# Kernel tuning notes

Hardware: AMD Instinct MI355X
Metric: run time of the kernel (lower is better)

## Reference

```python
import jax, jax.numpy as jnp
import numpy as np

N_HEADS = 32
N_KV_HEADS = 8
HEAD_DIM = 128
N_QUERY = N_HEADS // N_KV_HEADS  # 4
ROPE_BASE = 10000.0


def _rope_tables(seq_len, head_dim):
    # inv freqs over pairs of channels (Llama-style interleaved complex rotation)
    inv_freq = 1.0 / (ROPE_BASE ** (jnp.arange(0, head_dim, 2, dtype=jnp.float32) / head_dim))
    t = jnp.arange(seq_len, dtype=jnp.float32)
    ang = t[:, None] * inv_freq[None, :]           # [s, d/2]
    return jnp.cos(ang)[None, :, None, :], jnp.sin(ang)[None, :, None, :]  # [1,s,1,d/2]


def _apply_rope(x, cos, sin):
    # x: [b, s, h, d]; consecutive channel pairs are (real, imag)
    xr = x[..., 0::2]
    xi = x[..., 1::2]
    out_r = xr * cos - xi * sin
    out_i = xr * sin + xi * cos
    return jnp.stack([out_r, out_i], axis=-1).reshape(x.shape)


def setup_inputs() -> dict:
    key = jax.random.key(0)
    kx, kq, kk, kv, ko = jax.random.split(key, 5)
    dim = 4096
    kv_dim = N_KV_HEADS * HEAD_DIM
    scale = 0.02
    return {
        "x": jax.random.normal(kx, (2, 2048, dim), dtype=jnp.float32),
        "wq": jax.random.normal(kq, (dim, dim), dtype=jnp.float32) * scale,
        "wk": jax.random.normal(kk, (dim, kv_dim), dtype=jnp.float32) * scale,
        "wv": jax.random.normal(kv, (dim, kv_dim), dtype=jnp.float32) * scale,
        "wo": jax.random.normal(ko, (dim, dim), dtype=jnp.float32) * scale,
    }


def reference(x, wq, wk, wv, wo):
    b, s, _ = x.shape
    xq = (x @ wq).reshape(b, s, N_HEADS, HEAD_DIM)
    xk = (x @ wk).reshape(b, s, N_KV_HEADS, HEAD_DIM)
    xv = (x @ wv).reshape(b, s, N_KV_HEADS, HEAD_DIM)

    cos, sin = _rope_tables(s, HEAD_DIM)
    xq = _apply_rope(xq, cos, sin)
    xk = _apply_rope(xk, cos, sin)

    # GQA without materializing the KV expand: group query heads per kv head.
    qh = xq.reshape(b, s, N_KV_HEADS, N_QUERY, HEAD_DIM)
    scores = jnp.einsum('bsgnd,btgd->bgnst', qh, xk) / jnp.sqrt(
        jnp.asarray(HEAD_DIM, dtype=xq.dtype))  # [b,g,n,s,t]

    # causal mask: -inf above diagonal
    causal = jnp.arange(s)[:, None] >= jnp.arange(s)[None, :]
    scores = jnp.where(causal[None, None, None, :, :], scores, -jnp.inf)

    att = jax.nn.softmax(scores.astype(jnp.float32), axis=-1).astype(xq.dtype)
    out = jnp.einsum('bgnst,btgd->bsgnd', att, xv).reshape(b, s, N_HEADS * HEAD_DIM)
    return out @ wo
```

## Files before the change

kernel.cpp:

```cpp
#include <hip/hip_runtime.h>
#include <hip/hip_bf16.h>

typedef __attribute__((ext_vector_type(8))) short short8;
typedef __attribute__((ext_vector_type(4))) float f32x4;
typedef __attribute__((ext_vector_type(16))) float f32x16;

#define GLD16(gp, lp) __builtin_amdgcn_global_load_lds( \
    (const __attribute__((address_space(1))) unsigned int*)(gp), \
    (__attribute__((address_space(3))) unsigned int*)(lp), 16, 0, 0)

static __device__ __forceinline__ float bf2f(unsigned short u) {
    union { unsigned int i; float f; } v; v.i = ((unsigned int)u) << 16; return v.f;
}
static __device__ __forceinline__ short f2bf(float f) {
    union { float f; unsigned int i; } v; v.f = f;
    unsigned int r = v.i + 0x7FFFu + ((v.i >> 16) & 1u);
    return (short)(r >> 16);
}
static __device__ __forceinline__ unsigned int pack2bf(float lo, float hi) {
    return ((unsigned int)(unsigned short)f2bf(hi) << 16) | (unsigned int)(unsigned short)f2bf(lo);
}
static __device__ __forceinline__ unsigned int cvtpk(float lo, float hi) {
    unsigned int w;
    asm("v_cvt_pk_bf16_f32 %0, %1, %2" : "=v"(w) : "v"(lo), "v"(hi));
    return w;
}

__global__ void cast_f32_bf16(const float* __restrict__ src, short* __restrict__ dst, int n) {
    int i = (blockIdx.x * 256 + threadIdx.x) * 4;
    if (i >= n) return;
    float4 v = *(const float4*)(src + i);
    short4 o;
    o.x = f2bf(v.x); o.y = f2bf(v.y); o.z = f2bf(v.z); o.w = f2bf(v.w);
    *(short4*)(dst + i) = o;
}

__global__ void transpose_cast(const float* __restrict__ src, short* __restrict__ dst,
                               int N, int dstStride) {
    __shared__ float tile[32][33];
    int k0 = blockIdx.x * 32, n0 = blockIdx.y * 32;
    int t = threadIdx.x, c = t & 31, r = t >> 5;
#pragma unroll
    for (int p = 0; p < 4; ++p)
        tile[r + p * 8][c] = src[(size_t)(k0 + r + p * 8) * N + n0 + c];
    __syncthreads();
#pragma unroll
    for (int p = 0; p < 4; ++p)
        dst[(size_t)(n0 + r + p * 8) * dstStride + k0 + c] = f2bf(tile[c][r + p * 8]);
}

__global__ void transpose_v(const short* __restrict__ qkv, short* __restrict__ vt) {
    __shared__ short tile[32][33];
    int s0 = blockIdx.x * 32, d0 = blockIdx.y * 32;
    int bh = blockIdx.z;
    int b = bh >> 3, h = bh & 7;
    const short* src = qkv + (size_t)b * 2048 * 6144 + 5120 + h * 128;
    short* dst = vt + (size_t)bh * 128 * 2048;
    int t = threadIdx.x, c = t & 31, r = t >> 5;
#pragma unroll
    for (int p = 0; p < 4; ++p)
        tile[r + p * 8][c] = src[(size_t)(s0 + r + p * 8) * 6144 + d0 + c];
    __syncthreads();
#pragma unroll
    for (int p = 0; p < 4; ++p)
        dst[(size_t)(d0 + r + p * 8) * 2048 + s0 + c] = tile[c][r + p * 8];
}

__global__ void rope_tables(float* __restrict__ cs) {
    int i = blockIdx.x * 256 + threadIdx.x;
    int s = i >> 6, d2 = i & 63;
    float inv = expf(-9.210340371976184f * (float)(2 * d2) * (1.0f / 128.0f));
    float ang = (float)s * inv;
    float sn, c;
    sincosf(ang, &sn, &c);
    cs[(size_t)i * 2] = c;
    cs[(size_t)i * 2 + 1] = sn;
}

template<int NH>
__global__ void rope_apply(const short* __restrict__ qkv, const float* __restrict__ cs,
                           short* __restrict__ dst, int colOff, float scale) {
    int i = blockIdx.x * 256 + threadIdx.x;
    int d2 = i & 63;
    int t2 = i >> 6;
    int h = t2 % NH;
    int bs = t2 / NH;
    int s = bs & 2047;
    int b = bs >> 11;
    unsigned int pr = *(const unsigned int*)(qkv + (size_t)bs * 6144 + colOff + h * 128 + 2 * d2);
    float xr = bf2f((unsigned short)(pr & 0xFFFFu));
    float xi = bf2f((unsigned short)(pr >> 16));
    const float* cp = cs + ((size_t)s * 64 + d2) * 2;
    float c = cp[0], sn = cp[1];
    float outr = (xr * c - xi * sn) * scale;
    float outi = (xr * sn + xi * c) * scale;
    *(unsigned int*)(dst + ((size_t)(b * NH + h) * 2048 + s) * 128 + 2 * d2) = pack2bf(outr, outi);
}

template<bool BF16OUT>
__global__ __launch_bounds__(512, 1) void gemm256(const short* __restrict__ A,
                                                  const short* __restrict__ Bt,
                                                  void* __restrict__ Cv,
                                                  int Mtiles, int N, int K) {
    extern __shared__ __align__(16) short lds[];
    short* As = lds;
    short* Bs = lds + 32768;
    const int tid = threadIdx.x;
    const int lane = tid & 63;
    const int wid = tid >> 6;
    const int l31 = lane & 31;
    const int hi = lane >> 5;
    const int wr = wid >> 2;
    const int wc = wid & 3;

    const int nwg = gridDim.x;
    const int id = blockIdx.x;
    const int sid = (id & 7) * (nwg >> 3) + (id >> 3);
    const int m0 = (sid % Mtiles) * 256;
    const int n0 = (sid / Mtiles) * 256;

    const short* aBase = A + (size_t)m0 * K;
    const short* bBase = Bt + (size_t)n0 * K;
    const int NT = K >> 5;

    auto stage = [&](int t) {
        const int buf = t & 3;
        const short* as = aBase + t * 32;
        const short* bs = bBase + t * 32;
#pragma unroll
        for (int j = 0; j < 2; ++j) {
            int c = j * 512 + tid;
            int row = c >> 2;
            int sc = ((c & 3) ^ ((row >> 1) & 3)) * 8;
            GLD16(as + (size_t)row * K + sc, As + buf * 8192 + c * 8);
        }
#pragma unroll
        for (int j = 0; j < 2; ++j) {
            int c = j * 512 + tid;
            int row = c >> 2;
            int sc = ((c & 3) ^ ((row >> 1) & 3)) * 8;
            GLD16(bs + (size_t)row * K + sc, Bs + buf * 8192 + c * 8);
        }
    };

    f32x16 acc[4][2];
#pragma unroll
    for (int mi = 0; mi < 4; ++mi)
#pragma unroll
        for (int ni = 0; ni < 2; ++ni)
            acc[mi][ni] = f32x16{0,0,0,0,0,0,0,0,0,0,0,0,0,0,0,0};

    stage(0); stage(1); stage(2);
    asm volatile("s_waitcnt vmcnt(8)" ::: "memory");
    __builtin_amdgcn_sched_barrier(0);
    __builtin_amdgcn_s_barrier();
    __builtin_amdgcn_sched_barrier(0);

    for (int t = 0; t < NT; ++t) {
        const int buf = t & 3;
        if (t + 3 < NT) stage(t + 3);

        short8 af[4][2], bfr[2][2];
#pragma unroll
        for (int mi = 0; mi < 4; ++mi) {
            int row = wr * 128 + mi * 32 + l31;
            const short* rb = As + buf * 8192 + row * 32;
#pragma unroll
            for (int ks = 0; ks < 2; ++ks)
                af[mi][ks] = *(const short8*)(rb + (((ks * 2 + hi) ^ ((row >> 1) & 3)) * 8));
        }
#pragma unroll
        for (int ni = 0; ni < 2; ++ni) {
            int row = wc * 64 + ni * 32 + l31;
            const short* rb = Bs + buf * 8192 + row * 32;
#pragma unroll
            for (int ks = 0; ks < 2; ++ks)
                bfr[ni][ks] = *(const short8*)(rb + (((ks * 2 + hi) ^ ((row >> 1) & 3)) * 8));
        }

        __builtin_amdgcn_s_setprio(1);
#pragma unroll
        for (int ks = 0; ks < 2; ++ks)
#pragma unroll
            for (int mi = 0; mi < 4; ++mi)
#pragma unroll
                for (int ni = 0; ni < 2; ++ni)
                    acc[mi][ni] = __builtin_amdgcn_mfma_f32_32x32x16_bf16(af[mi][ks], bfr[ni][ks], acc[mi][ni], 0, 0, 0);
        __builtin_amdgcn_s_setprio(0);

        __builtin_amdgcn_sched_barrier(0);
        if (t + 3 < NT)       { asm volatile("s_waitcnt vmcnt(8)" ::: "memory"); }
        else if (t + 3 == NT) { asm volatile("s_waitcnt vmcnt(4)" ::: "memory"); }
        else if (t + 2 == NT) { asm volatile("s_waitcnt vmcnt(0)" ::: "memory"); }
        __builtin_amdgcn_sched_barrier(0);
        if (t + 1 < NT) {
            __builtin_amdgcn_s_barrier();
            __builtin_amdgcn_sched_barrier(0);
        }
    }

#pragma unroll
    for (int mi = 0; mi < 4; ++mi)
#pragma unroll
        for (int ni = 0; ni < 2; ++ni)
#pragma unroll
            for (int i = 0; i < 16; ++i) {
                int row = m0 + wr * 128 + mi * 32 + (i & 3) + 8 * (i >> 2) + 4 * hi;
                int col = n0 + wc * 64 + ni * 32 + l31;
                float v = acc[mi][ni][i];
                if constexpr (BF16OUT) ((short*)Cv)[(size_t)row * N + col] = f2bf(v);
                else                   ((float*)Cv)[(size_t)row * N + col] = v;
            }
}

__global__ __launch_bounds__(256, 2) void attn_kernel(const short* __restrict__ Qr,
                                                      const short* __restrict__ Kr,
                                                      const short* __restrict__ Vt,
                                                      short* __restrict__ Out) {
    __shared__ short Ks[64 * 128];
    __shared__ short Vs[128 * 64];
    const int qb = 15 - blockIdx.x;
    const int bh = blockIdx.y;
    const int b = bh >> 5;
    const int qh = bh & 31;
    const int kvh = qh >> 2;
    const int tid = threadIdx.x;
    const int lane = tid & 63;
    const int w = tid >> 6;
    const int l31 = lane & 31;
    const int hi = lane >> 5;
    const int qg0 = qb * 128 + w * 32;

    const short* qbase = Qr + ((size_t)bh * 2048 + qg0 + l31) * 128 + hi * 8;
    short8 qf[8];
#pragma unroll
    for (int ks = 0; ks < 8; ++ks)
        qf[ks] = *(const short8*)(qbase + ks * 16);

    const short* kbase = Kr + (size_t)(b * 8 + kvh) * 2048 * 128;
    const short* vbase = Vt + (size_t)(b * 8 + kvh) * 128 * 2048;

    float m_run = -INFINITY, l_run = 0.0f;
    f32x16 oacc[4];
#pragma unroll
    for (int dt = 0; dt < 4; ++dt) oacc[dt] = f32x16{0,0,0,0,0,0,0,0,0,0,0,0,0,0,0,0};

    const int nkb = 2 * qb + 2;
    for (int kb = 0; kb < nkb; ++kb) {
        const int s0 = kb * 64;
#pragma unroll
        for (int j = 0; j < 4; ++j) {
            int c = j * 256 + tid;
            int krow = c >> 4;
            int kcol = ((c & 15) ^ (krow & 7)) * 8;
            GLD16(kbase + (size_t)(s0 + krow) * 128 + kcol, Ks + (size_t)c * 8);
            int vrow = c >> 3;
            int vcol = ((c & 7) ^ (vrow & 7)) * 8;
            GLD16(vbase + (size_t)vrow * 2048 + s0 + vcol, Vs + (size_t)c * 8);
        }
        __syncthreads();

        if (s0 <= qg0 + 31) {
            f32x16 st0 = f32x16{0,0,0,0,0,0,0,0,0,0,0,0,0,0,0,0};
            f32x16 st1 = f32x16{0,0,0,0,0,0,0,0,0,0,0,0,0,0,0,0};
            __builtin_amdgcn_s_setprio(1);
#pragma unroll
            for (int ks = 0; ks < 8; ++ks) {
                int row0 = l31;
                int ch0 = ((2 * ks + hi) ^ (row0 & 7)) * 8;
                short8 kf0 = *(const short8*)(Ks + row0 * 128 + ch0);
                st0 = __builtin_amdgcn_mfma_f32_32x32x16_bf16(kf0, qf[ks], st0, 0, 0, 0);
                int row1 = 32 + l31;
                int ch1 = ((2 * ks + hi) ^ (row1 & 7)) * 8;
                short8 kf1 = *(const short8*)(Ks + row1 * 128 + ch1);
                st1 = __builtin_amdgcn_mfma_f32_32x32x16_bf16(kf1, qf[ks], st1, 0, 0, 0);
            }
            __builtin_amdgcn_s_setprio(0);

            const int q = qg0 + l31;
            if (s0 + 63 > qg0) {
#pragma unroll
                for (int i = 0; i < 16; ++i) {
                    int kvr = (i & 3) + 8 * (i >> 2) + 4 * hi;
                    if (s0 + kvr > q)      st0[i] = -INFINITY;
                    if (s0 + 32 + kvr > q) st1[i] = -INFINITY;
                }
            }

            float mx = -INFINITY;
#pragma unroll
            for (int i = 0; i < 16; ++i) mx = fmaxf(mx, fmaxf(st0[i], st1[i]));
            mx = fmaxf(mx, __shfl_xor(mx, 32, 64));

            const bool defer = __all(mx - m_run <= 8.0f);
            float mN, alpha;
            if (defer) { mN = m_run; alpha = 1.0f; }
            else       { mN = fmaxf(m_run, mx); alpha = __expf(m_run - mN); }

            float p0[16], p1[16];
            float rsum = 0.0f;
#pragma unroll
            for (int i = 0; i < 16; ++i) {
                p0[i] = __expf(st0[i] - mN);
                p1[i] = __expf(st1[i] - mN);
                rsum += p0[i] + p1[i];
            }
            rsum += __shfl_xor(rsum, 32, 64);
            l_run = l_run * alpha + rsum;
            m_run = mN;
            if (!defer) {
#pragma unroll
                for (int dt = 0; dt < 4; ++dt)
#pragma unroll
                    for (int i = 0; i < 16; ++i) oacc[dt][i] *= alpha;
            }

            short8 pfr[4];
#pragma unroll
            for (int kvs = 0; kvs < 4; ++kvs) {
                const float* pp = (kvs < 2) ? p0 : p1;
                const int h8 = (kvs & 1) * 8;
                unsigned int x0 = cvtpk(pp[h8 + 0], pp[h8 + 1]);
                unsigned int x1 = cvtpk(pp[h8 + 2], pp[h8 + 3]);
                unsigned int y0 = cvtpk(pp[h8 + 4], pp[h8 + 5]);
                unsigned int y1 = cvtpk(pp[h8 + 6], pp[h8 + 7]);
                asm("v_permlane32_swap_b32 %0, %1" : "+v"(x0), "+v"(y0));
                asm("v_permlane32_swap_b32 %0, %1" : "+v"(x1), "+v"(y1));
                union { unsigned int u[4]; short8 s; } uu;
                uu.u[0] = x0; uu.u[1] = x1; uu.u[2] = y0; uu.u[3] = y1;
                pfr[kvs] = uu.s;
            }

            __builtin_amdgcn_s_setprio(1);
#pragma unroll
            for (int dt = 0; dt < 4; ++dt) {
                int row = dt * 32 + l31;
#pragma unroll
                for (int kvs = 0; kvs < 4; ++kvs) {
                    int ch = ((2 * kvs + hi) ^ (row & 7)) * 8;
                    short8 vf = *(const short8*)(Vs + row * 64 + ch);
                    oacc[dt] = __builtin_amdgcn_mfma_f32_32x32x16_bf16(vf, pfr[kvs], oacc[dt], 0, 0, 0);
                }
            }
            __builtin_amdgcn_s_setprio(0);
        }
        __syncthreads();
    }

    const float inv = 1.0f / l_run;
    const size_t row = (size_t)b * 2048 + qg0 + l31;
    short* obase = Out + row * 4096 + qh * 128;
#pragma unroll
    for (int dt = 0; dt < 4; ++dt) {
#pragma unroll
        for (int g = 0; g < 4; ++g) {
            short4 o4;
            o4.x = f2bf(oacc[dt][g * 4 + 0] * inv);
            o4.y = f2bf(oacc[dt][g * 4 + 1] * inv);
            o4.z = f2bf(oacc[dt][g * 4 + 2] * inv);
            o4.w = f2bf(oacc[dt][g * 4 + 3] * inv);
            *(short4*)(obase + dt * 32 + g * 8 + hi * 4) = o4;
        }
    }
}


extern "C" void kernel_launch(void* const* d_in, const int* in_sizes, int n_in,
                              void* d_out, int out_size, void* d_ws, size_t ws_size,
                              hipStream_t stream) {
    const float* x  = (const float*)d_in[0];
    const float* wq = (const float*)d_in[1];
    const float* wk = (const float*)d_in[2];
    const float* wv = (const float*)d_in[3];
    const float* wo = (const float*)d_in[4];
    float* out = (float*)d_out;
    char* ws = (char*)d_ws;

    short* wt_qkv = (short*)(ws + 0);
    short* xb     = (short*)(ws + 50331648);
    short* qkv    = (short*)(ws + 83886080);
    short* wt_o   = (short*)(ws + 83886080);
    short* qr     = (short*)(ws + 134217728);
    short* kr     = (short*)(ws + 167772160);
    short* vt     = (short*)(ws + 176160768);
    float* tab    = (float*)(ws + 184549376);

    cast_f32_bf16<<<16384, 256, 0, stream>>>(x, xb, 16777216);
    transpose_cast<<<dim3(128, 128), 256, 0, stream>>>(wq, wt_qkv, 4096, 4096);
    transpose_cast<<<dim3(128, 32),  256, 0, stream>>>(wk, wt_qkv + (size_t)4096 * 4096, 1024, 4096);
    transpose_cast<<<dim3(128, 32),  256, 0, stream>>>(wv, wt_qkv + (size_t)5120 * 4096, 1024, 4096);
    rope_tables<<<512, 256, 0, stream>>>(tab);
    gemm256<true><<<384, 512, 131072, stream>>>(xb, wt_qkv, (void*)qkv, 16, 6144, 4096);
    rope_apply<32><<<32768, 256, 0, stream>>>(qkv, tab, qr, 0, 0.08838834764831845f);
    rope_apply<8><<<8192, 256, 0, stream>>>(qkv, tab, kr, 4096, 1.0f);
    transpose_v<<<dim3(64, 4, 16), 256, 0, stream>>>(qkv, vt);
    transpose_cast<<<dim3(128, 128), 256, 0, stream>>>(wo, wt_o, 4096, 4096);
    attn_kernel<<<dim3(16, 64), 256, 0, stream>>>(qr, kr, vt, xb);
    gemm256<false><<<256, 512, 131072, stream>>>(xb, wt_o, (void*)out, 16, 4096, 4096);
}
```

Before: 656.6 us.

## Switch GEMM to 16x16x32 MFMA with new LDS swizzle layout

```diff
diff --git a/kernel.cpp b/kernel.cpp
--- a/kernel.cpp
+++ b/kernel.cpp
@@ -108,8 +108,8 @@
     const int tid = threadIdx.x;
     const int lane = tid & 63;
     const int wid = tid >> 6;
-    const int l31 = lane & 31;
-    const int hi = lane >> 5;
+    const int lr = lane & 15;
+    const int lq = lane >> 4;
     const int wr = wid >> 2;
     const int wc = wid & 3;
 
@@ -125,30 +125,31 @@
 
     auto stage = [&](int t) {
         const int buf = t & 3;
-        const short* as = aBase + t * 32;
-        const short* bs = bBase + t * 32;
 #pragma unroll
         for (int j = 0; j < 2; ++j) {
-            int c = j * 512 + tid;
-            int row = c >> 2;
-            int sc = ((c & 3) ^ ((row >> 1) & 3)) * 8;
-            GLD16(as + (size_t)row * K + sc, As + buf * 8192 + c * 8);
+            int cl = j * 512 + tid;
+            int lrw = cl >> 3;
+            int cs = (cl & 7) ^ (lrw & 7);
+            int trow = lrw + ((cs & 4) << 5);
+            int kc = (cs & 3) * 8;
+            GLD16(aBase + (size_t)trow * K + t * 32 + kc, As + buf * 8192 + cl * 8);
         }
 #pragma unroll
         for (int j = 0; j < 2; ++j) {
-            int c = j * 512 + tid;
-            int row = c >> 2;
-            int sc = ((c & 3) ^ ((row >> 1) & 3)) * 8;
-            GLD16(bs + (size_t)row * K + sc, Bs + buf * 8192 + c * 8);
+            int cl = j * 512 + tid;
+            int lrw = cl >> 3;
+            int cs = (cl & 7) ^ (lrw & 7);
+            int trow = lrw + ((cs & 4) << 5);
+            int kc = (cs & 3) * 8;
+            GLD16(bBase + (size_t)trow * K + t * 32 + kc, Bs + buf * 8192 + cl * 8);
         }
     };
 
-    f32x16 acc[4][2];
-#pragma unroll
-    for (int mi = 0; mi < 4; ++mi)
-#pragma unroll
-        for (int ni = 0; ni < 2; ++ni)
-            acc[mi][ni] = f32x16{0,0,0,0,0,0,0,0,0,0,0,0,0,0,0,0};
+    f32x4 acc[8][4];
+#pragma unroll
+    for (int mi = 0; mi < 8; ++mi)
+#pragma unroll
+        for (int ni = 0; ni < 4; ++ni) acc[mi][ni] = f32x4{0.f, 0.f, 0.f, 0.f};
 
     stage(0); stage(1); stage(2);
     asm volatile("s_waitcnt vmcnt(8)" ::: "memory");
@@ -160,32 +161,27 @@
         const int buf = t & 3;
         if (t + 3 < NT) stage(t + 3);
 
-        short8 af[4][2], bfr[2][2];
-#pragma unroll
-        for (int mi = 0; mi < 4; ++mi) {
-            int row = wr * 128 + mi * 32 + l31;
-            const short* rb = As + buf * 8192 + row * 32;
-#pragma unroll
-            for (int ks = 0; ks < 2; ++ks)
-                af[mi][ks] = *(const short8*)(rb + (((ks * 2 + hi) ^ ((row >> 1) & 3)) * 8));
-        }
-#pragma unroll
-        for (int ni = 0; ni < 2; ++ni) {
-            int row = wc * 64 + ni * 32 + l31;
-            const short* rb = Bs + buf * 8192 + row * 32;
-#pragma unroll
-            for (int ks = 0; ks < 2; ++ks)
-                bfr[ni][ks] = *(const short8*)(rb + (((ks * 2 + hi) ^ ((row >> 1) & 3)) * 8));
+        short8 af[8], bfr[4];
+#pragma unroll
+        for (int mi = 0; mi < 8; ++mi) {
+            int lrw = (wr * 128 + mi * 16 + lr) & 127;
+            int chunk = ((wr << 2) | lq) ^ (lrw & 7);
+            af[mi] = *(const short8*)(As + buf * 8192 + lrw * 64 + chunk * 8);
+        }
+#pragma unroll
+        for (int ni = 0; ni < 4; ++ni) {
+            int tc = wc * 64 + ni * 16 + lr;
+            int lrw = tc & 127;
+            int chunk = (((tc >> 7) << 2) | lq) ^ (lrw & 7);
+            bfr[ni] = *(const short8*)(Bs + buf * 8192 + lrw * 64 + chunk * 8);
         }
 
         __builtin_amdgcn_s_setprio(1);
 #pragma unroll
-        for (int ks = 0; ks < 2; ++ks)
-#pragma unroll
-            for (int mi = 0; mi < 4; ++mi)
-#pragma unroll
-                for (int ni = 0; ni < 2; ++ni)
-                    acc[mi][ni] = __builtin_amdgcn_mfma_f32_32x32x16_bf16(af[mi][ks], bfr[ni][ks], acc[mi][ni], 0, 0, 0);
+        for (int mi = 0; mi < 8; ++mi)
+#pragma unroll
+            for (int ni = 0; ni < 4; ++ni)
+                acc[mi][ni] = __builtin_amdgcn_mfma_f32_16x16x32_bf16(af[mi], bfr[ni], acc[mi][ni], 0, 0, 0);
         __builtin_amdgcn_s_setprio(0);
 
         __builtin_amdgcn_sched_barrier(0);
@@ -200,14 +196,14 @@
     }
 
 #pragma unroll
-    for (int mi = 0; mi < 4; ++mi)
-#pragma unroll
-        for (int ni = 0; ni < 2; ++ni)
-#pragma unroll
-            for (int i = 0; i < 16; ++i) {
-                int row = m0 + wr * 128 + mi * 32 + (i & 3) + 8 * (i >> 2) + 4 * hi;
-                int col = n0 + wc * 64 + ni * 32 + l31;
-                float v = acc[mi][ni][i];
+    for (int mi = 0; mi < 8; ++mi)
+#pragma unroll
+        for (int ni = 0; ni < 4; ++ni)
+#pragma unroll
+            for (int r = 0; r < 4; ++r) {
+                int row = m0 + wr * 128 + mi * 16 + lq * 4 + r;
+                int col = n0 + wc * 64 + ni * 16 + lr;
+                float v = acc[mi][ni][r];
                 if constexpr (BF16OUT) ((short*)Cv)[(size_t)row * N + col] = f2bf(v);
                 else                   ((float*)Cv)[(size_t)row * N + col] = v;
             }
```

Result: faster. 617.9 us (-5.9%).
